# Optimization experiments

Measured on AMD Instinct MI355X. Metric: run time of the kernel, lower is better.

## Reference

```python
import jax, jax.numpy as jnp
import numpy as np

NEG_INF = -1e30


def setup_inputs() -> dict:
    B, N, D = 512, 256, 256
    key = jax.random.key(0)
    ks = jax.random.split(key, 10)
    s = 1.0 / np.sqrt(D)
    return {
        "enc": jax.random.normal(ks[0], (B, N, D), dtype=jnp.float32),
        "init_token": jax.random.normal(ks[1], (D,), dtype=jnp.float32),
        "w_ih": jax.random.uniform(ks[2], (3 * D, D), minval=-s, maxval=s, dtype=jnp.float32),
        "w_hh": jax.random.uniform(ks[3], (3 * D, D), minval=-s, maxval=s, dtype=jnp.float32),
        "b_ih": jax.random.uniform(ks[4], (3 * D,), minval=-s, maxval=s, dtype=jnp.float32),
        "b_hh": jax.random.uniform(ks[5], (3 * D,), minval=-s, maxval=s, dtype=jnp.float32),
        "wq": jax.random.uniform(ks[6], (D, D), minval=-s, maxval=s, dtype=jnp.float32),
        "bq": jax.random.uniform(ks[7], (D,), minval=-s, maxval=s, dtype=jnp.float32),
        "wk": jax.random.uniform(ks[8], (D, D), minval=-s, maxval=s, dtype=jnp.float32),
        "bk": jax.random.uniform(ks[9], (D,), minval=-s, maxval=s, dtype=jnp.float32),
    }


def gru_cell(x, h, w_ih, w_hh, b_ih, b_hh):
    # torch.nn.GRUCell math; gates packed as [reset, update, new]
    gi = x @ w_ih.T + b_ih          # [B, 3D]
    gh = h @ w_hh.T + b_hh          # [B, 3D]
    D = h.shape[-1]
    i_r, i_z, i_n = gi[:, :D], gi[:, D:2 * D], gi[:, 2 * D:]
    h_r, h_z, h_n = gh[:, :D], gh[:, D:2 * D], gh[:, 2 * D:]
    r = jax.nn.sigmoid(i_r + h_r)
    z = jax.nn.sigmoid(i_z + h_z)
    n = jnp.tanh(i_n + r * h_n)
    return (1.0 - z) * n + z * h


def pointer_decode(enc, init_token, w_ih, w_hh, b_ih, b_hh, wq, bq, wk, bk):
    # Greedy decode (deterministic analogue of decode_type='greedy').
    B, N, D = enc.shape
    scale = 1.0 / np.sqrt(D)
    keys = enc @ wk.T + bk                         # [B, N, D]
    rows = jnp.arange(B)

    def step(carry, _):
        state, prev_embed, mask = carry
        state = gru_cell(prev_embed, state, w_ih, w_hh, b_ih, b_hh)   # [B, D]
        query = state @ wq.T + bq                                     # [B, D]
        logits = jnp.einsum('bd,bnd->bn', query, keys) * scale        # [B, N]
        logits = jnp.where(mask, logits, NEG_INF)
        logp = jax.nn.log_softmax(logits, axis=-1)                    # [B, N]
        probs = jnp.exp(logp)
        entropy = -jnp.sum(probs * jnp.where(mask, logp, 0.0), axis=-1)  # [B]
        idx = jnp.argmax(probs, axis=-1)                              # [B]
        step_logp = logp[rows, idx]                                   # [B]
        prev_embed = enc[rows, idx]                                   # [B, D]
        mask = mask.at[rows, idx].set(False)
        return (state, prev_embed, mask), (idx, step_logp, entropy)

    carry0 = (enc.mean(axis=1),
              jnp.broadcast_to(init_token, (B, D)),
              jnp.ones((B, N), dtype=bool))
    _, (tours, logps, ents) = jax.lax.scan(step, carry0, None, length=N)
    return tours.T, logps.T, ents.T  # each [B, N]


def reference(enc, init_token, w_ih, w_hh, b_ih, b_hh, wq, bq, wk, bk):
    return pointer_decode(enc, init_token, w_ih, w_hh, b_ih, b_hh, wq, bq, wk, bk)
```

## Files before the change

### kernel.cpp

```cpp
#include <hip/hip_runtime.h>

#define B_ 512
#define N_ 256
#define D_ 256
#define NEGINF (-1e30)

typedef float v4f __attribute__((ext_vector_type(4)));

__device__ __forceinline__ v4f ntload4(const v4f* p) {
  return __builtin_nontemporal_load(p);
}

__global__ __launch_bounds__(256) void pack4C_k(const float* __restrict__ in,
                                                float* __restrict__ out, int R, int C) {
  int o = blockIdx.x * 256 + threadIdx.x;
  int total = R * (C >> 2);
  if (o >= total) return;
  int r = o % R, c4 = o / R;
  const float4 v = *(const float4*)(in + (size_t)r * C + c4 * 4);
  ((float4*)out)[o] = v;
}

__global__ __launch_bounds__(256) void wqk_k(const float* __restrict__ wk,
                                             const float* __restrict__ wq,
                                             const float* __restrict__ bq,
                                             double* __restrict__ Wqk,
                                             double* __restrict__ bqk) {
  int c = blockIdx.x, e = threadIdx.x;
  double acc = 0.0;
  for (int dd = 0; dd < 256; ++dd)
    acc += (double)wk[dd * 256 + c] * (double)wq[dd * 256 + e];
  Wqk[(e >> 1) * 512 + c * 2 + (e & 1)] = acc;
  if (e == 0) {
    double s = 0.0;
    for (int dd = 0; dd < 256; ++dd) s += (double)wk[dd * 256 + c] * (double)bq[dd];
    bqk[c] = s;
  }
}

__global__ __launch_bounds__(256) void encp_k(const float* __restrict__ enc,
                                              float* __restrict__ encP) {
  int b = blockIdx.y;
  int n0 = blockIdx.x * 64;
  int c = threadIdx.x;
  const float* src = enc + (size_t)b * 65536;
  float* dst = encP + (size_t)b * 65536;
  for (int k = 0; k < 64; ++k) {
    int n = n0 + k;
    dst[(c >> 2) * 1024 + n * 4 + (c & 3)] = src[n * 256 + c];
  }
}

__global__ __launch_bounds__(1024) void decode_k(
    const float* __restrict__ enc, const float* __restrict__ init_token,
    const float* __restrict__ b_ih, const float* __restrict__ b_hh,
    const float* __restrict__ wihP, const float* __restrict__ whhP,
    const double* __restrict__ Wqk, const double* __restrict__ bqk,
    const float* __restrict__ encP, float* __restrict__ out) {
  const int tid = threadIdx.x;
  const int s = tid >> 8;
  const int d = tid & 255;
  const int b0 = blockIdx.x * 2;

  __shared__ double a[2][4][1024];
  __shared__ double xS[2][D_], hS[2][D_];
  __shared__ double qs[2][D_];
  __shared__ double lg[2][N_];
  __shared__ unsigned char maskS[2][N_];
  __shared__ double redA[8], redB[8], redC[8];
  __shared__ int redI[8];

  const float* encB0 = enc + (size_t)b0 * 65536;
  const float* encB1 = encB0 + 65536;
  const v4f* encP0 = (const v4f*)encP + (size_t)b0 * 16384;
  const v4f* encP1 = encP0 + 16384;
  const v4f* wih4 = (const v4f*)wihP;
  const v4f* whh4 = (const v4f*)whhP;
  const double2* W2 = (const double2*)Wqk;

  {
    double p0 = 0.0, p1 = 0.0;
    const float* e0 = encB0 + (size_t)(s * 64) * 256 + d;
    const float* e1 = encB1 + (size_t)(s * 64) * 256 + d;
#pragma unroll 4
    for (int n = 0; n < 64; ++n) { p0 += (double)e0[n * 256]; p1 += (double)e1[n * 256]; }
    a[0][s][d] = p0;
    a[1][s][d] = p1;
  }
  __syncthreads();
  if (tid < 512) {
    int r = tid >> 8, j = tid & 255;
    hS[r][j] = (a[r][0][j] + a[r][1][j] + a[r][2][j] + a[r][3][j]) * (1.0 / 256.0);
    xS[r][j] = (double)init_token[j];
    maskS[r][j] = 1;
  }
  __syncthreads();

  for (int t = 0; t < N_; ++t) {
    {
      double pr0 = 0, pz0 = 0, pi0 = 0, ph0 = 0;
      double pr1 = 0, pz1 = 0, pi1 = 0, ph1 = 0;
      const int base = s * 16;
#pragma unroll 4
      for (int k = 0; k < 16; ++k) {
        int c4 = base + k;
        int wb = c4 * 768 + d;
        v4f wr = wih4[wb];
        v4f wz = wih4[wb + 256];
        v4f wn = wih4[wb + 512];
        v4f vr = whh4[wb];
        v4f vz = whh4[wb + 256];
        v4f vn = whh4[wb + 512];
        const double* x0 = &xS[0][c4 * 4];
        const double* h0 = &hS[0][c4 * 4];
        const double* x1 = &xS[1][c4 * 4];
        const double* h1 = &hS[1][c4 * 4];
#pragma unroll
        for (int i = 0; i < 4; ++i) {
          double wri = (double)wr[i], wzi = (double)wz[i], wni = (double)wn[i];
          double vri = (double)vr[i], vzi = (double)vz[i], vni = (double)vn[i];
          pr0 += wri * x0[i] + vri * h0[i];
          pz0 += wzi * x0[i] + vzi * h0[i];
          pi0 += wni * x0[i];
          ph0 += vni * h0[i];
          pr1 += wri * x1[i] + vri * h1[i];
          pz1 += wzi * x1[i] + vzi * h1[i];
          pi1 += wni * x1[i];
          ph1 += vni * h1[i];
        }
      }
      a[0][s][d] = pr0; a[0][s][256 + d] = pz0; a[0][s][512 + d] = pi0; a[0][s][768 + d] = ph0;
      a[1][s][d] = pr1; a[1][s][256 + d] = pz1; a[1][s][512 + d] = pi1; a[1][s][768 + d] = ph1;
    }
    __syncthreads();

    if (tid < 512) {
      int r = tid >> 8, j = tid & 255;
      double sr = a[r][0][j] + a[r][1][j] + a[r][2][j] + a[r][3][j]
                  + (double)b_ih[j] + (double)b_hh[j];
      double sz = a[r][0][256 + j] + a[r][1][256 + j] + a[r][2][256 + j] + a[r][3][256 + j]
                  + (double)b_ih[256 + j] + (double)b_hh[256 + j];
      double si = a[r][0][512 + j] + a[r][1][512 + j] + a[r][2][512 + j] + a[r][3][512 + j]
                  + (double)b_ih[512 + j];
      double sh = a[r][0][768 + j] + a[r][1][768 + j] + a[r][2][768 + j] + a[r][3][768 + j]
                  + (double)b_hh[512 + j];
      double rg = 1.0 / (1.0 + exp(-sr));
      double zg = 1.0 / (1.0 + exp(-sz));
      double nn = tanh(si + rg * sh);
      hS[r][j] = (1.0 - zg) * nn + zg * hS[r][j];
    }
    __syncthreads();

    {
      double q0 = (s == 0) ? bqk[d] : 0.0;
      double q1 = q0;
      const int e2b = s * 32;
#pragma unroll 4
      for (int k = 0; k < 32; ++k) {
        int e2 = e2b + k;
        double2 w = W2[e2 * 256 + d];
        q0 += w.x * hS[0][2 * e2] + w.y * hS[0][2 * e2 + 1];
        q1 += w.x * hS[1][2 * e2] + w.y * hS[1][2 * e2 + 1];
      }
      a[0][s][d] = q0;
      a[1][s][d] = q1;
    }
    __syncthreads();

    if (tid < 512) {
      int r = tid >> 8, j = tid & 255;
      qs[r][j] = a[r][0][j] + a[r][1][j] + a[r][2][j] + a[r][3][j];
    }
    __syncthreads();

    {
      double p0 = 0, p1 = 0;
      const int base = s * 16;
#pragma unroll 2
      for (int k = 0; k < 16; ++k) {
        int c4 = base + k;
        v4f k0 = ntload4(encP0 + c4 * 256 + d);
        v4f k1 = ntload4(encP1 + c4 * 256 + d);
        const double* q0p = &qs[0][c4 * 4];
        const double* q1p = &qs[1][c4 * 4];
#pragma unroll
        for (int i = 0; i < 4; ++i) {
          p0 += (double)k0[i] * q0p[i];
          p1 += (double)k1[i] * q1p[i];
        }
      }
      a[0][s][d] = p0;
      a[1][s][d] = p1;
    }
    __syncthreads();

    double lgv = NEGINF, mR = NEGINF;
    int amax = 0;
    if (tid < 512) {
      int r = tid >> 8, n = tid & 255;
      lgv = 0.0625 * (a[r][0][n] + a[r][1][n] + a[r][2][n] + a[r][3][n]);
      if (!maskS[r][n]) lgv = NEGINF;
      lg[r][n] = lgv;
      double v = lgv;
      int idx = n;
#pragma unroll
      for (int off = 32; off > 0; off >>= 1) {
        double ov = __shfl_down(v, off);
        int oi = __shfl_down(idx, off);
        if (ov > v || (ov == v && oi < idx)) { v = ov; idx = oi; }
      }
      if ((tid & 63) == 0) { redA[tid >> 6] = v; redI[tid >> 6] = idx; }
    }
    __syncthreads();

    if (tid < 512) {
      int r = tid >> 8, n = tid & 255;
      double bv = redA[r * 4];
      int bi = redI[r * 4];
#pragma unroll
      for (int w = 1; w < 4; ++w) {
        double wv = redA[r * 4 + w];
        int wi2 = redI[r * 4 + w];
        if (wv > bv || (wv == bv && wi2 < bi)) { bv = wv; bi = wi2; }
      }
      mR = bv;
      amax = bi;
      double e = exp(lgv - mR);
      double t2 = e * (lgv - mR);
      double s1 = e, s2 = t2;
#pragma unroll
      for (int off = 32; off > 0; off >>= 1) {
        s1 += __shfl_down(s1, off);
        s2 += __shfl_down(s2, off);
      }
      if ((tid & 63) == 0) { redB[tid >> 6] = s1; redC[tid >> 6] = s2; }
      const float* encR = (r == 0) ? encB0 : encB1;
      xS[r][n] = (double)__builtin_nontemporal_load(encR + (size_t)amax * 256 + n);
    }
    __syncthreads();

    if (tid < 512 && (tid & 255) == 0) {
      int r = tid >> 8;
      double S1 = redB[r * 4] + redB[r * 4 + 1] + redB[r * 4 + 2] + redB[r * 4 + 3];
      double S2 = redC[r * 4] + redC[r * 4 + 1] + redC[r * 4 + 2] + redC[r * 4 + 3];
      double lS = log(S1);
      double logZ = mR + lS;
      size_t row = (size_t)(b0 + r) * N_;
      out[row + t] = (float)amax;
      out[(size_t)B_ * N_ + row + t] = (float)(lg[r][amax] - logZ);
      out[2 * (size_t)B_ * N_ + row + t] = (float)(lS - S2 / S1);
      maskS[r][amax] = 0;
    }
    __syncthreads();
  }
}

extern "C" void kernel_launch(void* const* d_in, const int* in_sizes, int n_in,
                              void* d_out, int out_size, void* d_ws, size_t ws_size,
                              hipStream_t stream) {
  const float* enc = (const float*)d_in[0];
  const float* init_token = (const float*)d_in[1];
  const float* w_ih = (const float*)d_in[2];
  const float* w_hh = (const float*)d_in[3];
  const float* b_ih = (const float*)d_in[4];
  const float* b_hh = (const float*)d_in[5];
  const float* wq = (const float*)d_in[6];
  const float* bq = (const float*)d_in[7];
  const float* wk = (const float*)d_in[8];
  const float* bk = (const float*)d_in[9];
  (void)bk;
  float* out = (float*)d_out;
  char* wsb = (char*)d_ws;

  float* wihP = (float*)(wsb + 0);
  float* whhP = (float*)(wsb + 786432);
  double* Wqk = (double*)(wsb + 1572864);
  double* bqk = (double*)(wsb + 2097152);
  float* encP = (float*)(wsb + 2099200);

  hipLaunchKernelGGL(pack4C_k, dim3(192), dim3(256), 0, stream, w_ih, wihP, 768, 256);
  hipLaunchKernelGGL(pack4C_k, dim3(192), dim3(256), 0, stream, w_hh, whhP, 768, 256);
  hipLaunchKernelGGL(wqk_k, dim3(256), dim3(256), 0, stream, wk, wq, bq, Wqk, bqk);
  hipLaunchKernelGGL(encp_k, dim3(4, 512), dim3(256), 0, stream, enc, encP);
  hipLaunchKernelGGL(decode_k, dim3(B_ / 2), dim3(1024), 0, stream, enc, init_token,
                     b_ih, b_hh, wihP, whhP, Wqk, bqk, encP, out);
}
```

Before: 13.88 ms.

## Precompute input-gate projections for all nodes and restructure decode with wave-level reductions

Adds a kernel that computes enc @ w_ih^T + b_ih for every batch row and node ahead of the loop and stores it in double precision. Each decode step then gathers the selected node's row instead of doing the x-side GRU matvec, which removes half of the recurrent matvec work from the sequential loop. The weight, encoder and Wqk layouts are repacked so that four lanes split each output's dot product and combine it with xor shuffles. This drops the shared-memory partial-sum arrays and several barriers per step. The trade-off is a large workspace buffer (about 800MB of doubles) and extra precompute traffic, with a fallback path used when the workspace is too small.

```diff
diff --git a/kernel.cpp b/kernel.cpp
--- a/kernel.cpp
+++ b/kernel.cpp
@@ -7,30 +7,42 @@
 
 typedef float v4f __attribute__((ext_vector_type(4)));
 
-__device__ __forceinline__ v4f ntload4(const v4f* p) {
-  return __builtin_nontemporal_load(p);
-}
-
-__global__ __launch_bounds__(256) void pack4C_k(const float* __restrict__ in,
-                                                float* __restrict__ out, int R, int C) {
-  int o = blockIdx.x * 256 + threadIdx.x;
-  int total = R * (C >> 2);
-  if (o >= total) return;
-  int r = o % R, c4 = o / R;
-  const float4 v = *(const float4*)(in + (size_t)r * C + c4 * 4);
-  ((float4*)out)[o] = v;
+__global__ void transpose_k(const float* __restrict__ in, float* __restrict__ out,
+                            int R, int C) {
+  __shared__ float tile[32][33];
+  int rb = blockIdx.y * 32, cb = blockIdx.x * 32;
+  int tx = threadIdx.x, ty = threadIdx.y;
+  for (int i = ty; i < 32; i += 8) {
+    int r = rb + i, c = cb + tx;
+    if (r < R && c < C) tile[i][tx] = in[r * C + c];
+  }
+  __syncthreads();
+  for (int i = ty; i < 32; i += 8) {
+    int c = cb + i, r = rb + tx;
+    if (r < R && c < C) out[c * R + r] = tile[tx][i];
+  }
+}
+
+__global__ __launch_bounds__(256) void packW_k(const float* __restrict__ in,
+                                               float* __restrict__ out) {
+  int idx = blockIdx.x * 256 + threadIdx.x;
+  int j = idx >> 6, c4 = idx & 63;
+  int g = j >> 8, o = j & 255;
+  int w16 = o >> 4, k = c4 & 15, l = 4 * (o & 15) + (c4 >> 4);
+  ((v4f*)out)[((w16 * 16 + k) * 3 + g) * 64 + l] = ((const v4f*)in)[idx];
 }
 
 __global__ __launch_bounds__(256) void wqk_k(const float* __restrict__ wk,
                                              const float* __restrict__ wq,
                                              const float* __restrict__ bq,
-                                             double* __restrict__ Wqk,
+                                             double* __restrict__ WqkP,
                                              double* __restrict__ bqk) {
   int c = blockIdx.x, e = threadIdx.x;
   double acc = 0.0;
   for (int dd = 0; dd < 256; ++dd)
     acc += (double)wk[dd * 256 + c] * (double)wq[dd * 256 + e];
-  Wqk[(e >> 1) * 512 + c * 2 + (e & 1)] = acc;
+  int w16 = c >> 4, k2 = (e >> 1) & 31, l = 4 * (c & 15) + (e >> 6), comp = e & 1;
+  WqkP[(size_t)(((w16 * 32) + k2) * 64 + l) * 2 + comp] = acc;
   if (e == 0) {
     double s = 0.0;
     for (int dd = 0; dd < 256; ++dd) s += (double)wk[dd * 256 + c] * (double)bq[dd];
@@ -41,217 +53,296 @@
 __global__ __launch_bounds__(256) void encp_k(const float* __restrict__ enc,
                                               float* __restrict__ encP) {
   int b = blockIdx.y;
-  int n0 = blockIdx.x * 64;
-  int c = threadIdx.x;
-  const float* src = enc + (size_t)b * 65536;
-  float* dst = encP + (size_t)b * 65536;
-  for (int k = 0; k < 64; ++k) {
-    int n = n0 + k;
-    dst[(c >> 2) * 1024 + n * 4 + (c & 3)] = src[n * 256 + c];
-  }
-}
-
-__global__ __launch_bounds__(1024) void decode_k(
+  int idx = blockIdx.x * 256 + threadIdx.x;
+  int l = idx & 63, rest = idx >> 6;
+  int k = rest & 15, w16 = rest >> 4;
+  int n = w16 * 16 + (l >> 2), c4 = (l & 3) * 16 + k;
+  ((v4f*)encP)[(size_t)b * 16384 + idx] =
+      *(const v4f*)(enc + (size_t)b * 65536 + n * 256 + c4 * 4);
+}
+
+__global__ __launch_bounds__(768) void gi_k(const float* __restrict__ enc,
+                                            const float* __restrict__ wihT,
+                                            const float* __restrict__ b_ih,
+                                            double* __restrict__ Gi) {
+  int b = blockIdx.x, j = threadIdx.x;
+  __shared__ float encS[32][256];
+  const float* encB = enc + (size_t)b * 65536;
+  double bias = (double)b_ih[j];
+  for (int n0 = 0; n0 < 256; n0 += 32) {
+    __syncthreads();
+    for (int i = j; i < 2048; i += 768)
+      ((float4*)encS)[i] = ((const float4*)(encB + n0 * 256))[i];
+    __syncthreads();
+    double acc[32];
+#pragma unroll
+    for (int jj = 0; jj < 32; ++jj) acc[jj] = bias;
+    for (int c0 = 0; c0 < 256; c0 += 4) {
+      double w0 = (double)wihT[(c0 + 0) * 768 + j];
+      double w1 = (double)wihT[(c0 + 1) * 768 + j];
+      double w2 = (double)wihT[(c0 + 2) * 768 + j];
+      double w3 = (double)wihT[(c0 + 3) * 768 + j];
+#pragma unroll
+      for (int jj = 0; jj < 32; ++jj) {
+        const float4 e = *(const float4*)&encS[jj][c0];
+        acc[jj] += w0 * (double)e.x + w1 * (double)e.y + w2 * (double)e.z + w3 * (double)e.w;
+      }
+    }
+#pragma unroll
+    for (int jj = 0; jj < 32; ++jj)
+      Gi[((size_t)b * 256 + n0 + jj) * 768 + j] = acc[jj];
+  }
+}
+
+template <bool USE_GI>
+__global__ __launch_bounds__(1024, 4) void decode_k(
     const float* __restrict__ enc, const float* __restrict__ init_token,
     const float* __restrict__ b_ih, const float* __restrict__ b_hh,
     const float* __restrict__ wihP, const float* __restrict__ whhP,
-    const double* __restrict__ Wqk, const double* __restrict__ bqk,
-    const float* __restrict__ encP, float* __restrict__ out) {
+    const double* __restrict__ WqkP, const double* __restrict__ bqk,
+    const float* __restrict__ encP, const double* __restrict__ Gi,
+    float* __restrict__ out) {
   const int tid = threadIdx.x;
-  const int s = tid >> 8;
-  const int d = tid & 255;
+  const int WV = tid >> 6;
+  const int LN = tid & 63;
+  const int O = WV * 16 + (LN >> 2);
+  const int S = LN & 3;
+  const int ROW = S >> 1;
   const int b0 = blockIdx.x * 2;
 
-  __shared__ double a[2][4][1024];
-  __shared__ double xS[2][D_], hS[2][D_];
-  __shared__ double qs[2][D_];
+  __shared__ alignas(16) double hS[2][2][D_];
+  __shared__ alignas(16) double xS[2][D_];
+  __shared__ alignas(16) double giS[2][768];
+  __shared__ alignas(16) double qs[2][D_];
   __shared__ double lg[2][N_];
   __shared__ unsigned char maskS[2][N_];
-  __shared__ double redA[8], redB[8], redC[8];
-  __shared__ int redI[8];
+  __shared__ double redA[16][2], redB[16][2], redC[16][2];
+  __shared__ int redI[16][2];
 
   const float* encB0 = enc + (size_t)b0 * 65536;
   const float* encB1 = encB0 + 65536;
-  const v4f* encP0 = (const v4f*)encP + (size_t)b0 * 16384;
-  const v4f* encP1 = encP0 + 16384;
-  const v4f* wih4 = (const v4f*)wihP;
-  const v4f* whh4 = (const v4f*)whhP;
-  const double2* W2 = (const double2*)Wqk;
-
+  const v4f* eP0 = (const v4f*)encP + (size_t)b0 * 16384;
+  const v4f* eP1 = eP0 + 16384;
+  const v4f* wh4 = (const v4f*)whhP;
+  const v4f* wi4 = (const v4f*)wihP;
+  const double2* Wp2 = (const double2*)WqkP;
+
+  if (tid < 256) xS[0][tid] = (double)init_token[tid];
   {
     double p0 = 0.0, p1 = 0.0;
-    const float* e0 = encB0 + (size_t)(s * 64) * 256 + d;
-    const float* e1 = encB1 + (size_t)(s * 64) * 256 + d;
+    const float* e0 = encB0 + (size_t)(S * 64) * 256 + O;
+    const float* e1 = encB1 + (size_t)(S * 64) * 256 + O;
 #pragma unroll 4
     for (int n = 0; n < 64; ++n) { p0 += (double)e0[n * 256]; p1 += (double)e1[n * 256]; }
-    a[0][s][d] = p0;
-    a[1][s][d] = p1;
-  }
+    p0 += __shfl_xor(p0, 1); p0 += __shfl_xor(p0, 2);
+    p1 += __shfl_xor(p1, 1); p1 += __shfl_xor(p1, 2);
+    if (S == 0) { hS[0][0][O] = p0 * (1.0 / 256.0); hS[0][1][O] = p1 * (1.0 / 256.0); }
+  }
+  if (tid < 256) { maskS[0][tid] = 1; maskS[1][tid] = 1; }
   __syncthreads();
-  if (tid < 512) {
-    int r = tid >> 8, j = tid & 255;
-    hS[r][j] = (a[r][0][j] + a[r][1][j] + a[r][2][j] + a[r][3][j]) * (1.0 / 256.0);
-    xS[r][j] = (double)init_token[j];
-    maskS[r][j] = 1;
+  if (USE_GI) {
+    double a0 = 0, a1 = 0, a2 = 0;
+#pragma unroll 2
+    for (int k = 0; k < 16; ++k) {
+      int wb = ((WV * 16 + k) * 3) * 64 + LN;
+      v4f ar = wi4[wb], az = wi4[wb + 64], an = wi4[wb + 128];
+      const double* xp = &xS[0][S * 64 + 4 * k];
+#pragma unroll
+      for (int i = 0; i < 4; ++i) {
+        a0 += (double)ar[i] * xp[i];
+        a1 += (double)az[i] * xp[i];
+        a2 += (double)an[i] * xp[i];
+      }
+    }
+    a0 += __shfl_xor(a0, 1); a0 += __shfl_xor(a0, 2);
+    a1 += __shfl_xor(a1, 1); a1 += __shfl_xor(a1, 2);
+    a2 += __shfl_xor(a2, 1); a2 += __shfl_xor(a2, 2);
+    if (S == 0) {
+      double v0 = a0 + (double)b_ih[O];
+      double v1 = a1 + (double)b_ih[256 + O];
+      double v2 = a2 + (double)b_ih[512 + O];
+      giS[0][O] = v0;        giS[1][O] = v0;
+      giS[0][256 + O] = v1;  giS[1][256 + O] = v1;
+      giS[0][512 + O] = v2;  giS[1][512 + O] = v2;
+    }
+  } else {
+    if (tid < 256) xS[1][tid] = xS[0][tid];
   }
   __syncthreads();
 
+  int cur = 0;
   for (int t = 0; t < N_; ++t) {
+    const int nxt = cur ^ 1;
+    double ghr0 = 0, ghz0 = 0, ghn0 = 0, ghr1 = 0, ghz1 = 0, ghn1 = 0;
+    double air0 = 0, aiz0 = 0, ain0 = 0, air1 = 0, aiz1 = 0, ain1 = 0;
+#pragma unroll 2
+    for (int k = 0; k < 16; ++k) {
+      int wb = ((WV * 16 + k) * 3) * 64 + LN;
+      v4f br = wh4[wb], bz = wh4[wb + 64], bn = wh4[wb + 128];
+      int c = S * 64 + 4 * k;
+      const double* h0 = &hS[cur][0][c];
+      const double* h1 = &hS[cur][1][c];
+#pragma unroll
+      for (int i = 0; i < 4; ++i) {
+        double wr = (double)br[i], wz = (double)bz[i], wn = (double)bn[i];
+        ghr0 += wr * h0[i]; ghz0 += wz * h0[i]; ghn0 += wn * h0[i];
+        ghr1 += wr * h1[i]; ghz1 += wz * h1[i]; ghn1 += wn * h1[i];
+      }
+      if (!USE_GI) {
+        v4f ar = wi4[wb], az = wi4[wb + 64], an = wi4[wb + 128];
+        const double* x0 = &xS[0][c];
+        const double* x1 = &xS[1][c];
+#pragma unroll
+        for (int i = 0; i < 4; ++i) {
+          double wr = (double)ar[i], wz = (double)az[i], wn = (double)an[i];
+          air0 += wr * x0[i]; aiz0 += wz * x0[i]; ain0 += wn * x0[i];
+          air1 += wr * x1[i]; aiz1 += wz * x1[i]; ain1 += wn * x1[i];
+        }
+      }
+    }
+    ghr0 += __shfl_xor(ghr0, 1); ghr0 += __shfl_xor(ghr0, 2);
+    ghz0 += __shfl_xor(ghz0, 1); ghz0 += __shfl_xor(ghz0, 2);
+    ghn0 += __shfl_xor(ghn0, 1); ghn0 += __shfl_xor(ghn0, 2);
+    ghr1 += __shfl_xor(ghr1, 1); ghr1 += __shfl_xor(ghr1, 2);
+    ghz1 += __shfl_xor(ghz1, 1); ghz1 += __shfl_xor(ghz1, 2);
+    ghn1 += __shfl_xor(ghn1, 1); ghn1 += __shfl_xor(ghn1, 2);
+    if (!USE_GI) {
+      air0 += __shfl_xor(air0, 1); air0 += __shfl_xor(air0, 2);
+      aiz0 += __shfl_xor(aiz0, 1); aiz0 += __shfl_xor(aiz0, 2);
+      ain0 += __shfl_xor(ain0, 1); ain0 += __shfl_xor(ain0, 2);
+      air1 += __shfl_xor(air1, 1); air1 += __shfl_xor(air1, 2);
+      aiz1 += __shfl_xor(aiz1, 1); aiz1 += __shfl_xor(aiz1, 2);
+      ain1 += __shfl_xor(ain1, 1); ain1 += __shfl_xor(ain1, 2);
+    }
     {
-      double pr0 = 0, pz0 = 0, pi0 = 0, ph0 = 0;
-      double pr1 = 0, pz1 = 0, pi1 = 0, ph1 = 0;
-      const int base = s * 16;
-#pragma unroll 4
-      for (int k = 0; k < 16; ++k) {
-        int c4 = base + k;
-        int wb = c4 * 768 + d;
-        v4f wr = wih4[wb];
-        v4f wz = wih4[wb + 256];
-        v4f wn = wih4[wb + 512];
-        v4f vr = whh4[wb];
-        v4f vz = whh4[wb + 256];
-        v4f vn = whh4[wb + 512];
-        const double* x0 = &xS[0][c4 * 4];
-        const double* h0 = &hS[0][c4 * 4];
-        const double* x1 = &xS[1][c4 * 4];
-        const double* h1 = &hS[1][c4 * 4];
-#pragma unroll
-        for (int i = 0; i < 4; ++i) {
-          double wri = (double)wr[i], wzi = (double)wz[i], wni = (double)wn[i];
-          double vri = (double)vr[i], vzi = (double)vz[i], vni = (double)vn[i];
-          pr0 += wri * x0[i] + vri * h0[i];
-          pz0 += wzi * x0[i] + vzi * h0[i];
-          pi0 += wni * x0[i];
-          ph0 += vni * h0[i];
-          pr1 += wri * x1[i] + vri * h1[i];
-          pz1 += wzi * x1[i] + vzi * h1[i];
-          pi1 += wni * x1[i];
-          ph1 += vni * h1[i];
-        }
-      }
-      a[0][s][d] = pr0; a[0][s][256 + d] = pz0; a[0][s][512 + d] = pi0; a[0][s][768 + d] = ph0;
-      a[1][s][d] = pr1; a[1][s][256 + d] = pz1; a[1][s][512 + d] = pi1; a[1][s][768 + d] = ph1;
-    }
-    __syncthreads();
-
-    if (tid < 512) {
-      int r = tid >> 8, j = tid & 255;
-      double sr = a[r][0][j] + a[r][1][j] + a[r][2][j] + a[r][3][j]
-                  + (double)b_ih[j] + (double)b_hh[j];
-      double sz = a[r][0][256 + j] + a[r][1][256 + j] + a[r][2][256 + j] + a[r][3][256 + j]
-                  + (double)b_ih[256 + j] + (double)b_hh[256 + j];
-      double si = a[r][0][512 + j] + a[r][1][512 + j] + a[r][2][512 + j] + a[r][3][512 + j]
-                  + (double)b_ih[512 + j];
-      double sh = a[r][0][768 + j] + a[r][1][768 + j] + a[r][2][768 + j] + a[r][3][768 + j]
-                  + (double)b_hh[512 + j];
-      double rg = 1.0 / (1.0 + exp(-sr));
-      double zg = 1.0 / (1.0 + exp(-sz));
-      double nn = tanh(si + rg * sh);
-      hS[r][j] = (1.0 - zg) * nn + zg * hS[r][j];
+      double gir, giz, gin;
+      if (USE_GI) {
+        gir = giS[ROW][O]; giz = giS[ROW][256 + O]; gin = giS[ROW][512 + O];
+      } else {
+        gir = (ROW ? air1 : air0) + (double)b_ih[O];
+        giz = (ROW ? aiz1 : aiz0) + (double)b_ih[256 + O];
+        gin = (ROW ? ain1 : ain0) + (double)b_ih[512 + O];
+      }
+      double hr_ = (ROW ? ghr1 : ghr0) + (double)b_hh[O];
+      double hz_ = (ROW ? ghz1 : ghz0) + (double)b_hh[256 + O];
+      double hn_ = (ROW ? ghn1 : ghn0) + (double)b_hh[512 + O];
+      double rr = 1.0 / (1.0 + exp(-(gir + hr_)));
+      double zz = 1.0 / (1.0 + exp(-(giz + hz_)));
+      double nn = tanh(gin + rr * hn_);
+      double hold = hS[cur][ROW][O];
+      double hnew = (1.0 - zz) * nn + zz * hold;
+      if ((S & 1) == 0) hS[nxt][ROW][O] = hnew;
     }
     __syncthreads();
 
     {
-      double q0 = (s == 0) ? bqk[d] : 0.0;
-      double q1 = q0;
-      const int e2b = s * 32;
+      double q0 = 0, q1 = 0;
 #pragma unroll 4
       for (int k = 0; k < 32; ++k) {
-        int e2 = e2b + k;
-        double2 w = W2[e2 * 256 + d];
-        q0 += w.x * hS[0][2 * e2] + w.y * hS[0][2 * e2 + 1];
-        q1 += w.x * hS[1][2 * e2] + w.y * hS[1][2 * e2 + 1];
-      }
-      a[0][s][d] = q0;
-      a[1][s][d] = q1;
-    }
-    __syncthreads();
-
-    if (tid < 512) {
-      int r = tid >> 8, j = tid & 255;
-      qs[r][j] = a[r][0][j] + a[r][1][j] + a[r][2][j] + a[r][3][j];
-    }
-    __syncthreads();
-
+        double2 wv = Wp2[(WV * 32 + k) * 64 + LN];
+        int dd = S * 64 + 2 * k;
+        q0 += wv.x * hS[nxt][0][dd] + wv.y * hS[nxt][0][dd + 1];
+        q1 += wv.x * hS[nxt][1][dd] + wv.y * hS[nxt][1][dd + 1];
+      }
+      q0 += __shfl_xor(q0, 1); q0 += __shfl_xor(q0, 2);
+      q1 += __shfl_xor(q1, 1); q1 += __shfl_xor(q1, 2);
+      if (S == 0) { double bb = bqk[O]; qs[0][O] = q0 + bb; qs[1][O] = q1 + bb; }
+    }
+    __syncthreads();
+
+    double lgv0, lgv1;
     {
       double p0 = 0, p1 = 0;
-      const int base = s * 16;
 #pragma unroll 2
       for (int k = 0; k < 16; ++k) {
-        int c4 = base + k;
-        v4f k0 = ntload4(encP0 + c4 * 256 + d);
-        v4f k1 = ntload4(encP1 + c4 * 256 + d);
-        const double* q0p = &qs[0][c4 * 4];
-        const double* q1p = &qs[1][c4 * 4];
+        int eb = (WV * 16 + k) * 64 + LN;
+        v4f e0 = eP0[eb];
+        v4f e1 = eP1[eb];
+        int c = S * 64 + 4 * k;
+        const double* qa = &qs[0][c];
+        const double* qb = &qs[1][c];
 #pragma unroll
         for (int i = 0; i < 4; ++i) {
-          p0 += (double)k0[i] * q0p[i];
-          p1 += (double)k1[i] * q1p[i];
+          p0 += (double)e0[i] * qa[i];
+          p1 += (double)e1[i] * qb[i];
         }
       }
-      a[0][s][d] = p0;
-      a[1][s][d] = p1;
-    }
-    __syncthreads();
-
-    double lgv = NEGINF, mR = NEGINF;
-    int amax = 0;
-    if (tid < 512) {
-      int r = tid >> 8, n = tid & 255;
-      lgv = 0.0625 * (a[r][0][n] + a[r][1][n] + a[r][2][n] + a[r][3][n]);
-      if (!maskS[r][n]) lgv = NEGINF;
-      lg[r][n] = lgv;
-      double v = lgv;
-      int idx = n;
-#pragma unroll
-      for (int off = 32; off > 0; off >>= 1) {
-        double ov = __shfl_down(v, off);
-        int oi = __shfl_down(idx, off);
-        if (ov > v || (ov == v && oi < idx)) { v = ov; idx = oi; }
-      }
-      if ((tid & 63) == 0) { redA[tid >> 6] = v; redI[tid >> 6] = idx; }
-    }
-    __syncthreads();
-
-    if (tid < 512) {
-      int r = tid >> 8, n = tid & 255;
-      double bv = redA[r * 4];
-      int bi = redI[r * 4];
-#pragma unroll
-      for (int w = 1; w < 4; ++w) {
-        double wv = redA[r * 4 + w];
-        int wi2 = redI[r * 4 + w];
-        if (wv > bv || (wv == bv && wi2 < bi)) { bv = wv; bi = wi2; }
-      }
-      mR = bv;
-      amax = bi;
-      double e = exp(lgv - mR);
-      double t2 = e * (lgv - mR);
-      double s1 = e, s2 = t2;
-#pragma unroll
-      for (int off = 32; off > 0; off >>= 1) {
-        s1 += __shfl_down(s1, off);
-        s2 += __shfl_down(s2, off);
-      }
-      if ((tid & 63) == 0) { redB[tid >> 6] = s1; redC[tid >> 6] = s2; }
-      const float* encR = (r == 0) ? encB0 : encB1;
-      xS[r][n] = (double)__builtin_nontemporal_load(encR + (size_t)amax * 256 + n);
-    }
-    __syncthreads();
-
-    if (tid < 512 && (tid & 255) == 0) {
-      int r = tid >> 8;
-      double S1 = redB[r * 4] + redB[r * 4 + 1] + redB[r * 4 + 2] + redB[r * 4 + 3];
-      double S2 = redC[r * 4] + redC[r * 4 + 1] + redC[r * 4 + 2] + redC[r * 4 + 3];
+      p0 += __shfl_xor(p0, 1); p0 += __shfl_xor(p0, 2);
+      p1 += __shfl_xor(p1, 1); p1 += __shfl_xor(p1, 2);
+      lgv0 = 0.0625 * p0; if (!maskS[0][O]) lgv0 = NEGINF;
+      lgv1 = 0.0625 * p1; if (!maskS[1][O]) lgv1 = NEGINF;
+      if (S == 0) { lg[0][O] = lgv0; lg[1][O] = lgv1; }
+      double v0 = lgv0, v1 = lgv1;
+      int i0 = O, i1 = O;
+#pragma unroll
+      for (int off = 1; off < 64; off <<= 1) {
+        double t0 = __shfl_xor(v0, off); int ti0 = __shfl_xor(i0, off);
+        if (t0 > v0 || (t0 == v0 && ti0 < i0)) { v0 = t0; i0 = ti0; }
+        double t1 = __shfl_xor(v1, off); int ti1 = __shfl_xor(i1, off);
+        if (t1 > v1 || (t1 == v1 && ti1 < i1)) { v1 = t1; i1 = ti1; }
+      }
+      if (LN == 0) { redA[WV][0] = v0; redI[WV][0] = i0; redA[WV][1] = v1; redI[WV][1] = i1; }
+    }
+    __syncthreads();
+
+    double m0 = -1e300, m1 = -1e300;
+    int am0 = 0, am1 = 0;
+#pragma unroll 4
+    for (int w = 0; w < 16; ++w) {
+      double va = redA[w][0]; int ia = redI[w][0];
+      if (va > m0 || (va == m0 && ia < am0)) { m0 = va; am0 = ia; }
+      double vb = redA[w][1]; int ib = redI[w][1];
+      if (vb > m1 || (vb == m1 && ib < am1)) { m1 = vb; am1 = ib; }
+    }
+    {
+      double e0 = (S == 0) ? exp(lgv0 - m0) : 0.0;
+      double e1 = (S == 0) ? exp(lgv1 - m1) : 0.0;
+      double s20 = e0 * (lgv0 - m0);
+      double s21 = e1 * (lgv1 - m1);
+#pragma unroll
+      for (int off = 1; off < 64; off <<= 1) {
+        e0 += __shfl_xor(e0, off);
+        e1 += __shfl_xor(e1, off);
+        s20 += __shfl_xor(s20, off);
+        s21 += __shfl_xor(s21, off);
+      }
+      if (LN == 0) { redB[WV][0] = e0; redB[WV][1] = e1; redC[WV][0] = s20; redC[WV][1] = s21; }
+    }
+    if (USE_GI) {
+      size_t g0 = ((size_t)b0 * 256 + am0) * 768;
+      size_t g1 = ((size_t)(b0 + 1) * 256 + am1) * 768;
+      if (tid < 768) giS[0][tid] = Gi[g0 + tid];
+      int t2 = tid - 256;
+      if (t2 >= 0 && t2 < 768) giS[1][t2] = Gi[g1 + t2];
+    } else {
+      if (tid < 512) {
+        int r = tid >> 8, j = tid & 255;
+        int am = r ? am1 : am0;
+        int c4 = j >> 2;
+        int vidx = ((am >> 4) * 16 + (c4 & 15)) * 64 + (4 * (am & 15) + (c4 >> 4));
+        const float* ePr = r ? (const float*)eP1 : (const float*)eP0;
+        xS[r][j] = (double)ePr[vidx * 4 + (j & 3)];
+      }
+    }
+    __syncthreads();
+
+    if (tid < 2) {
+      int r = tid;
+      double m = r ? m1 : m0;
+      int am = r ? am1 : am0;
+      double S1 = 0, S2 = 0;
+#pragma unroll 4
+      for (int w = 0; w < 16; ++w) { S1 += redB[w][r]; S2 += redC[w][r]; }
       double lS = log(S1);
-      double logZ = mR + lS;
+      double logZ = m + lS;
       size_t row = (size_t)(b0 + r) * N_;
-      out[row + t] = (float)amax;
-      out[(size_t)B_ * N_ + row + t] = (float)(lg[r][amax] - logZ);
+      out[row + t] = (float)am;
+      out[(size_t)B_ * N_ + row + t] = (float)(lg[r][am] - logZ);
       out[2 * (size_t)B_ * N_ + row + t] = (float)(lS - S2 / S1);
-      maskS[r][amax] = 0;
-    }
-    __syncthreads();
+      maskS[r][am] = 0;
+    }
+    __syncthreads();
+    cur ^= 1;
   }
 }
 
@@ -274,14 +365,24 @@
 
   float* wihP = (float*)(wsb + 0);
   float* whhP = (float*)(wsb + 786432);
-  double* Wqk = (double*)(wsb + 1572864);
+  double* WqkP = (double*)(wsb + 1572864);
   double* bqk = (double*)(wsb + 2097152);
   float* encP = (float*)(wsb + 2099200);
-
-  hipLaunchKernelGGL(pack4C_k, dim3(192), dim3(256), 0, stream, w_ih, wihP, 768, 256);
-  hipLaunchKernelGGL(pack4C_k, dim3(192), dim3(256), 0, stream, w_hh, whhP, 768, 256);
-  hipLaunchKernelGGL(wqk_k, dim3(256), dim3(256), 0, stream, wk, wq, bq, Wqk, bqk);
-  hipLaunchKernelGGL(encp_k, dim3(4, 512), dim3(256), 0, stream, enc, encP);
-  hipLaunchKernelGGL(decode_k, dim3(B_ / 2), dim3(1024), 0, stream, enc, init_token,
-                     b_ih, b_hh, wihP, whhP, Wqk, bqk, encP, out);
-}
+  float* wihT = (float*)(wsb + 136316928);
+  double* Gi = (double*)(wsb + 137103360);
+  const bool useGi = ws_size >= 942409728ull;
+
+  hipLaunchKernelGGL(packW_k, dim3(192), dim3(256), 0, stream, w_ih, wihP);
+  hipLaunchKernelGGL(packW_k, dim3(192), dim3(256), 0, stream, w_hh, whhP);
+  hipLaunchKernelGGL(wqk_k, dim3(256), dim3(256), 0, stream, wk, wq, bq, WqkP, bqk);
+  hipLaunchKernelGGL(encp_k, dim3(64, 512), dim3(256), 0, stream, enc, encP);
+  if (useGi) {
+    hipLaunchKernelGGL(transpose_k, dim3(8, 24), dim3(32, 8), 0, stream, w_ih, wihT, 768, 256);
+    hipLaunchKernelGGL(gi_k, dim3(512), dim3(768), 0, stream, enc, wihT, b_ih, Gi);
+    hipLaunchKernelGGL(decode_k<true>, dim3(B_ / 2), dim3(1024), 0, stream, enc, init_token,
+                       b_ih, b_hh, wihP, whhP, WqkP, bqk, encP, Gi, out);
+  } else {
+    hipLaunchKernelGGL(decode_k<false>, dim3(B_ / 2), dim3(1024), 0, stream, enc, init_token,
+                       b_ih, b_hh, wihP, whhP, WqkP, bqk, encP, Gi, out);
+  }
+}
```

Result: slower. 17.32 ms (+24.8%).
